# Performance work log

Measured on AMD Instinct MI355X. Metric: run time of the kernel, lower is better.

The kernel has to match this reference:

```python
import jax, jax.numpy as jnp
import numpy as np
from math import sqrt

NOISE_STD = 0.05
ALPHA = 0.2
RHO = 1.0
B, T, I, H, O, R = 64, 2048, 3, 512, 1, 1


def setup_inputs() -> dict:
    key = jax.random.key(0)
    ks = jax.random.split(key, 8)
    return {
        'input': jax.random.normal(ks[0], (B, T, I), dtype=jnp.float32),
        'noise': jax.random.normal(ks[1], (B, T, H), dtype=jnp.float32),
        'w_i': jax.random.normal(ks[2], (I, H), dtype=jnp.float32),
        's_i': jnp.ones((I,), dtype=jnp.float32),
        'm_rec': jax.random.normal(ks[3], (H, R), dtype=jnp.float32),
        'n_rec': jax.random.normal(ks[4], (H, R), dtype=jnp.float32),
        'rec_noise': jax.random.normal(ks[5], (H, H), dtype=jnp.float32) * (RHO / sqrt(H)),
        'w_o': jax.random.normal(ks[6], (H, O), dtype=jnp.float32),
        's_o': jnp.ones((O,), dtype=jnp.float32),
        'h0': jnp.zeros((H,), dtype=jnp.float32),
    }


def reference(input, noise, w_i, s_i, m_rec, n_rec, rec_noise, w_o, s_o, h0):
    hidden = h0.shape[0]
    # proxy parameters (define_proxy_parameters)
    w_rec = m_rec @ n_rec.T / hidden + rec_noise          # [H, H]
    wi_full = w_i * s_i[:, None]                          # [I, H]
    wo_full = w_o * s_o                                   # [H, O]
    # per-step additive drive: noise_std*noise + alpha * (input @ wi_full)
    drive = NOISE_STD * noise + ALPHA * jnp.einsum('bti,ih->bth', input, wi_full)  # [B,T,H]
    h_init = jnp.broadcast_to(h0, (input.shape[0], hidden))

    def step(h, d_t):
        r = jnp.tanh(h)
        h_new = h + d_t + ALPHA * (-h + r @ w_rec.T)
        return h_new, jnp.tanh(h_new)

    _, r_seq = jax.lax.scan(step, h_init, jnp.swapaxes(drive, 0, 1))  # r_seq: [T,B,H]
    output = jnp.einsum('tbh,ho->bto', r_seq, wo_full) / hidden        # [B,T,O]
    return output
```

## Files before the change

kernel.cpp:

```cpp
#include <hip/hip_runtime.h>

constexpr int Bc = 64;
constexpr int Tc = 2048;
constexpr int Ic = 3;
constexpr int Hc = 512;
constexpr float AL = 0.2f;
constexpr float NS = 0.05f;
constexpr int NSL = 4;
constexpr int HS  = Hc / NSL;
constexpr int PAD = 132;

__global__ void prep_wt(const float* __restrict__ m, const float* __restrict__ n,
                        const float* __restrict__ rn, float* __restrict__ WT, int R) {
    int id = blockIdx.x * 256 + threadIdx.x;
    if (id >= Hc * Hc) return;
    int k = id >> 9;
    int h = id & (Hc - 1);
    float acc = rn[h * Hc + k];
    for (int r = 0; r < R; ++r)
        acc = fmaf(m[h * R + r], n[k * R + r] * (1.0f / Hc), acc);
    WT[id] = acc;
}

__device__ __forceinline__ unsigned long long ld_sc0(const unsigned long long* p) {
    unsigned long long v;
    asm volatile("global_load_dwordx2 %0, %1, off sc0\n\t"
                 "s_waitcnt vmcnt(0)"
                 : "=v"(v) : "v"(p) : "memory");
    return v;
}

#define REPEAT32(F) F(0) F(1) F(2) F(3) F(4) F(5) F(6) F(7) \
                    F(8) F(9) F(10) F(11) F(12) F(13) F(14) F(15) \
                    F(16) F(17) F(18) F(19) F(20) F(21) F(22) F(23) \
                    F(24) F(25) F(26) F(27) F(28) F(29) F(30) F(31)

#define WDECL(i) float4 w##i;
#define WLOAD(i) w##i = make_float4(Wp[(size_t)(4*(i)+0) * Hc], \
                                    Wp[(size_t)(4*(i)+1) * Hc], \
                                    Wp[(size_t)(4*(i)+2) * Hc], \
                                    Wp[(size_t)(4*(i)+3) * Hc]);
#define WPIN(i)  asm volatile("" : "+v"(w##i.x), "+v"(w##i.y), "+v"(w##i.z), "+v"(w##i.w));
#define WFMA(i)  { const float4 rv##i = *(const float4*)(rg + 4*(i)); \
                   acc0 = fmaf(w##i.x, rv##i.x, acc0); \
                   acc1 = fmaf(w##i.y, rv##i.y, acc1); \
                   acc2 = fmaf(w##i.z, rv##i.z, acc2); \
                   acc3 = fmaf(w##i.w, rv##i.w, acc3); }

__launch_bounds__(512, 2)
__global__ void rnn4r(const float* __restrict__ input, const float* __restrict__ noise,
                      const float* __restrict__ w_i, const float* __restrict__ s_i,
                      const float* __restrict__ WT, const float* __restrict__ w_o,
                      const float* __restrict__ s_o, const float* __restrict__ h0,
                      float* __restrict__ out, unsigned long long* __restrict__ rbuf) {
    __shared__ float rp[2][NSL * PAD];
    __shared__ float red[8];

    const int tid   = threadIdx.x;
    const int s     = blockIdx.x >> 6;
    const int b     = blockIdx.x & 63;
    const int hl    = tid >> 2;
    const int kg    = tid & 3;
    const int hbase = s * HS;
    const int hmy   = hbase + hl;

    const float* Wp = WT + (size_t)(kg * 128) * Hc + hmy;
    REPEAT32(WDECL)
    REPEAT32(WLOAD)
    REPEAT32(WPIN)

    const float wo_t = w_o[tid] * s_o[0] * (1.0f / Hc);
    float h = h0[hmy];
    const float wi0 = w_i[0 * Hc + hmy] * s_i[0];
    const float wi1 = w_i[1 * Hc + hmy] * s_i[1];
    const float wi2 = w_i[2 * Hc + hmy] * s_i[2];

    rp[0][(tid >> 7) * PAD + (tid & 127)] = tanhf(h0[tid]);

    const float* noise_b = noise + (size_t)b * Tc * Hc;
    const float* inp_b   = input + (size_t)b * Tc * Ic;
    unsigned long long* rb_b = rbuf + (size_t)b * 2 * Hc;

    float nz = noise_b[hmy];
    float i0 = inp_b[0], i1 = inp_b[1], i2 = inp_b[2];

    const int ft   = tid + ((tid >= hbase) ? 128 : 0);
    const int fpos = (ft >> 7) * PAD + (ft & 127);
    __syncthreads();

    for (int t = 0; t < Tc; ++t) {
        const int tn = (t + 1 < Tc) ? t + 1 : t;
        const float nz_n = noise_b[(size_t)tn * Hc + hmy];
        const float i0n = inp_b[tn * Ic + 0];
        const float i1n = inp_b[tn * Ic + 1];
        const float i2n = inp_b[tn * Ic + 2];

        const float* rg = &rp[t & 1][kg * PAD];
        float acc0 = 0.f, acc1 = 0.f, acc2 = 0.f, acc3 = 0.f;
        REPEAT32(WFMA)
        float y = (acc0 + acc1) + (acc2 + acc3);
        y += __shfl_xor(y, 1, 64);
        y += __shfl_xor(y, 2, 64);

        const float di = i0 * wi0 + i1 * wi1 + i2 * wi2;
        h = h + (NS * nz + AL * di) + AL * (y - h);
        const float rv_ = tanhf(h);

        const unsigned want = (unsigned)(t + 1);
        unsigned long long* slot = rb_b + ((size_t)((t + 1) & 1)) * Hc;
        float* wp_ = &rp[(t + 1) & 1][0];

        if (kg == 0) {
            __hip_atomic_store(&slot[hmy],
                               ((unsigned long long)want << 32) |
                               (unsigned long long)__float_as_uint(rv_),
                               __ATOMIC_RELAXED, __HIP_MEMORY_SCOPE_AGENT);
            wp_[s * PAD + hl] = rv_;
        }

        if (tid < 384) {
            const unsigned long long* p = &slot[ft];
            unsigned long long v;
            int it = 0;
            for (;;) {
                if ((it & 3) != 3)
                    v = ld_sc0(p);
                else
                    v = __hip_atomic_load(p, __ATOMIC_RELAXED, __HIP_MEMORY_SCOPE_AGENT);
                if ((unsigned)(v >> 32) == want) break;
                ++it;
            }
            wp_[fpos] = __uint_as_float((unsigned)v);
        }
        __syncthreads();

        if ((t & 3) == s) {
            float p2 = wp_[(tid >> 7) * PAD + (tid & 127)] * wo_t;
            #pragma unroll
            for (int off = 32; off; off >>= 1) p2 += __shfl_xor(p2, off, 64);
            if ((tid & 63) == 0) red[tid >> 6] = p2;
            __syncthreads();
            if (tid == 0)
                out[(size_t)b * Tc + t] = red[0] + red[1] + red[2] + red[3] +
                                          red[4] + red[5] + red[6] + red[7];
        }

        nz = nz_n; i0 = i0n; i1 = i1n; i2 = i2n;
    }
}

__launch_bounds__(512)
__global__ void rnn_scan_fb(const float* __restrict__ input, const float* __restrict__ noise,
                            const float* __restrict__ w_i, const float* __restrict__ s_i,
                            const float* __restrict__ WT, const float* __restrict__ w_o,
                            const float* __restrict__ s_o, const float* __restrict__ h0,
                            float* __restrict__ out) {
    __shared__ float r_lds[Hc];
    __shared__ float pl[4][Hc];
    __shared__ float wi_lds[Ic][Hc];
    __shared__ float red[8];

    const int tid = threadIdx.x;
    const int b   = blockIdx.x;
    const int g   = tid >> 7;
    const int j   = tid & 127;

    for (int i = 0; i < Ic; ++i) wi_lds[i][tid] = w_i[i * Hc + tid] * s_i[i];

    float h = h0[tid];
    float r_cur = tanhf(h);
    const float wo_h = w_o[tid] * s_o[0] * (1.0f / Hc);
    const float* noise_b = noise + (size_t)b * Tc * Hc;
    const float* inp_b   = input + (size_t)b * Tc * Ic;
    float nz = noise_b[tid];
    float i0 = inp_b[0], i1 = inp_b[1], i2 = inp_b[2];
    const float* Wg = WT + (g * 128) * Hc + 4 * j;
    const float* rg = r_lds + g * 128;
    __syncthreads();

    for (int t = 0; t < Tc; ++t) {
        const int tn = (t + 1 < Tc) ? t + 1 : t;
        const float nz_n = noise_b[(size_t)tn * Hc + tid];
        const float i0n = inp_b[tn * Ic + 0];
        const float i1n = inp_b[tn * Ic + 1];
        const float i2n = inp_b[tn * Ic + 2];

        r_lds[tid] = r_cur;
        __syncthreads();
        float a0 = 0.f, a1 = 0.f, a2 = 0.f, a3 = 0.f;
        #pragma unroll 4
        for (int kk = 0; kk < 128; kk += 4) {
            const float4 rv = *(const float4*)(rg + kk);
            const float4 w0 = *(const float4*)(Wg + (kk + 0) * Hc);
            const float4 w1 = *(const float4*)(Wg + (kk + 1) * Hc);
            const float4 w2 = *(const float4*)(Wg + (kk + 2) * Hc);
            const float4 w3 = *(const float4*)(Wg + (kk + 3) * Hc);
            a0 = fmaf(rv.x, w0.x, a0); a0 = fmaf(rv.y, w1.x, a0);
            a0 = fmaf(rv.z, w2.x, a0); a0 = fmaf(rv.w, w3.x, a0);
            a1 = fmaf(rv.x, w0.y, a1); a1 = fmaf(rv.y, w1.y, a1);
            a1 = fmaf(rv.z, w2.y, a1); a1 = fmaf(rv.w, w3.y, a1);
            a2 = fmaf(rv.x, w0.z, a2); a2 = fmaf(rv.y, w1.z, a2);
            a2 = fmaf(rv.z, w2.z, a2); a2 = fmaf(rv.w, w3.z, a2);
            a3 = fmaf(rv.x, w0.w, a3); a3 = fmaf(rv.y, w1.w, a3);
            a3 = fmaf(rv.z, w2.w, a3); a3 = fmaf(rv.w, w3.w, a3);
        }
        *(float4*)&pl[g][4 * j] = make_float4(a0, a1, a2, a3);
        __syncthreads();

        const float y  = pl[0][tid] + pl[1][tid] + pl[2][tid] + pl[3][tid];
        const float di = i0 * wi_lds[0][tid] + i1 * wi_lds[1][tid] + i2 * wi_lds[2][tid];
        h = h + (NS * nz + AL * di) + AL * (y - h);
        r_cur = tanhf(h);

        float p = r_cur * wo_h;
        #pragma unroll
        for (int off = 32; off; off >>= 1) p += __shfl_xor(p, off, 64);
        if ((tid & 63) == 0) red[tid >> 6] = p;
        __syncthreads();
        if (tid == 0)
            out[(size_t)b * Tc + t] = red[0] + red[1] + red[2] + red[3] +
                                      red[4] + red[5] + red[6] + red[7];
        nz = nz_n; i0 = i0n; i1 = i1n; i2 = i2n;
    }
}

extern "C" void kernel_launch(void* const* d_in, const int* in_sizes, int n_in,
                              void* d_out, int out_size, void* d_ws, size_t ws_size,
                              hipStream_t stream) {
    (void)n_in; (void)out_size;
    const float* input     = (const float*)d_in[0];
    const float* noise     = (const float*)d_in[1];
    const float* w_i       = (const float*)d_in[2];
    const float* s_i       = (const float*)d_in[3];
    const float* m_rec     = (const float*)d_in[4];
    const float* n_rec     = (const float*)d_in[5];
    const float* rec_noise = (const float*)d_in[6];
    const float* w_o       = (const float*)d_in[7];
    const float* s_o       = (const float*)d_in[8];
    const float* h0        = (const float*)d_in[9];
    float* out = (float*)d_out;

    const int R = in_sizes[4] / Hc;

    float* WT = (float*)d_ws;
    const size_t wt_bytes = (size_t)Hc * Hc * sizeof(float);
    const size_t rb_bytes = (size_t)Bc * 2 * Hc * sizeof(unsigned long long);

    prep_wt<<<(Hc * Hc + 255) / 256, 256, 0, stream>>>(m_rec, n_rec, rec_noise, WT, R);

    if (ws_size >= wt_bytes + rb_bytes) {
        unsigned long long* rbuf = (unsigned long long*)((char*)d_ws + wt_bytes);
        hipMemsetAsync(rbuf, 0, rb_bytes, stream);
        rnn4r<<<NSL * Bc, 512, 0, stream>>>(input, noise, w_i, s_i, WT, w_o, s_o, h0,
                                            out, rbuf);
    } else {
        rnn_scan_fb<<<Bc, 512, 0, stream>>>(input, noise, w_i, s_i, WT, w_o, s_o, h0, out);
    }
}
```

Baseline: 3.812 ms.

## Split recurrent matvec K dimension across 8 lanes with 1024-thread blocks

Each block now uses 1024 threads, with 8 lanes per hidden unit instead of 4, so each lane holds 64 weights in registers instead of 128 and does half the FMAs per step. The aim is to shorten the per-step critical path of the recurrence and reduce register pressure. The cost is an extra shuffle reduction stage, twice as many waves per barrier, and a reshaped LDS layout with different padding. Occupancy is pinned to 4 waves per EU, which allows one block per CU.

```diff
diff --git a/kernel.cpp b/kernel.cpp
--- a/kernel.cpp
+++ b/kernel.cpp
@@ -7,8 +7,10 @@
 constexpr float AL = 0.2f;
 constexpr float NS = 0.05f;
 constexpr int NSL = 4;
-constexpr int HS  = Hc / NSL;
-constexpr int PAD = 132;
+constexpr int HS  = 128;
+constexpr int KG  = 8;
+constexpr int KS  = 64;
+constexpr int SLP = 68;
 
 __global__ void prep_wt(const float* __restrict__ m, const float* __restrict__ n,
                         const float* __restrict__ rn, float* __restrict__ WT, int R) {
@@ -30,10 +32,8 @@
     return v;
 }
 
-#define REPEAT32(F) F(0) F(1) F(2) F(3) F(4) F(5) F(6) F(7) \
-                    F(8) F(9) F(10) F(11) F(12) F(13) F(14) F(15) \
-                    F(16) F(17) F(18) F(19) F(20) F(21) F(22) F(23) \
-                    F(24) F(25) F(26) F(27) F(28) F(29) F(30) F(31)
+#define REPEAT16(F) F(0) F(1) F(2) F(3) F(4) F(5) F(6) F(7) \
+                    F(8) F(9) F(10) F(11) F(12) F(13) F(14) F(15)
 
 #define WDECL(i) float4 w##i;
 #define WLOAD(i) w##i = make_float4(Wp[(size_t)(4*(i)+0) * Hc], \
@@ -47,35 +47,39 @@
                    acc2 = fmaf(w##i.z, rv##i.z, acc2); \
                    acc3 = fmaf(w##i.w, rv##i.w, acc3); }
 
-__launch_bounds__(512, 2)
-__global__ void rnn4r(const float* __restrict__ input, const float* __restrict__ noise,
-                      const float* __restrict__ w_i, const float* __restrict__ s_i,
-                      const float* __restrict__ WT, const float* __restrict__ w_o,
-                      const float* __restrict__ s_o, const float* __restrict__ h0,
-                      float* __restrict__ out, unsigned long long* __restrict__ rbuf) {
-    __shared__ float rp[2][NSL * PAD];
+__global__ __launch_bounds__(1024)
+__attribute__((amdgpu_waves_per_eu(4, 4)))
+void rnn8g(const float* __restrict__ input, const float* __restrict__ noise,
+           const float* __restrict__ w_i, const float* __restrict__ s_i,
+           const float* __restrict__ WT, const float* __restrict__ w_o,
+           const float* __restrict__ s_o, const float* __restrict__ h0,
+           float* __restrict__ out, unsigned long long* __restrict__ rbuf) {
+    __shared__ __align__(16) float rp[2][KG * SLP];
     __shared__ float red[8];
 
     const int tid   = threadIdx.x;
     const int s     = blockIdx.x >> 6;
     const int b     = blockIdx.x & 63;
-    const int hl    = tid >> 2;
-    const int kg    = tid & 3;
+    const int hl    = tid >> 3;
+    const int kg    = tid & 7;
     const int hbase = s * HS;
     const int hmy   = hbase + hl;
 
-    const float* Wp = WT + (size_t)(kg * 128) * Hc + hmy;
-    REPEAT32(WDECL)
-    REPEAT32(WLOAD)
-    REPEAT32(WPIN)
-
-    const float wo_t = w_o[tid] * s_o[0] * (1.0f / Hc);
+    const float* Wp = WT + (size_t)(kg * KS) * Hc + hmy;
+    REPEAT16(WDECL)
+    REPEAT16(WLOAD)
+    REPEAT16(WPIN)
+
     float h = h0[hmy];
     const float wi0 = w_i[0 * Hc + hmy] * s_i[0];
     const float wi1 = w_i[1 * Hc + hmy] * s_i[1];
     const float wi2 = w_i[2 * Hc + hmy] * s_i[2];
 
-    rp[0][(tid >> 7) * PAD + (tid & 127)] = tanhf(h0[tid]);
+    float wo_t = 0.f;
+    if (tid < Hc) {
+        wo_t = w_o[tid] * s_o[0] * (1.0f / Hc);
+        rp[0][(tid >> 6) * SLP + (tid & 63)] = tanhf(h0[tid]);
+    }
 
     const float* noise_b = noise + (size_t)b * Tc * Hc;
     const float* inp_b   = input + (size_t)b * Tc * Ic;
@@ -84,8 +88,8 @@
     float nz = noise_b[hmy];
     float i0 = inp_b[0], i1 = inp_b[1], i2 = inp_b[2];
 
-    const int ft   = tid + ((tid >= hbase) ? 128 : 0);
-    const int fpos = (ft >> 7) * PAD + (ft & 127);
+    const int ft   = tid + ((tid >= hbase) ? HS : 0);
+    const int fpos = (ft >> 6) * SLP + (ft & 63);
     __syncthreads();
 
     for (int t = 0; t < Tc; ++t) {
@@ -95,12 +99,13 @@
         const float i1n = inp_b[tn * Ic + 1];
         const float i2n = inp_b[tn * Ic + 2];
 
-        const float* rg = &rp[t & 1][kg * PAD];
+        const float* rg = &rp[t & 1][kg * SLP];
         float acc0 = 0.f, acc1 = 0.f, acc2 = 0.f, acc3 = 0.f;
-        REPEAT32(WFMA)
+        REPEAT16(WFMA)
         float y = (acc0 + acc1) + (acc2 + acc3);
         y += __shfl_xor(y, 1, 64);
         y += __shfl_xor(y, 2, 64);
+        y += __shfl_xor(y, 4, 64);
 
         const float di = i0 * wi0 + i1 * wi1 + i2 * wi2;
         h = h + (NS * nz + AL * di) + AL * (y - h);
@@ -115,7 +120,7 @@
                                ((unsigned long long)want << 32) |
                                (unsigned long long)__float_as_uint(rv_),
                                __ATOMIC_RELAXED, __HIP_MEMORY_SCOPE_AGENT);
-            wp_[s * PAD + hl] = rv_;
+            wp_[(hmy >> 6) * SLP + (hmy & 63)] = rv_;
         }
 
         if (tid < 384) {
@@ -135,10 +140,10 @@
         __syncthreads();
 
         if ((t & 3) == s) {
-            float p2 = wp_[(tid >> 7) * PAD + (tid & 127)] * wo_t;
+            float p2 = (tid < Hc) ? wp_[(tid >> 6) * SLP + (tid & 63)] * wo_t : 0.f;
             #pragma unroll
             for (int off = 32; off; off >>= 1) p2 += __shfl_xor(p2, off, 64);
-            if ((tid & 63) == 0) red[tid >> 6] = p2;
+            if (tid < Hc && (tid & 63) == 0) red[tid >> 6] = p2;
             __syncthreads();
             if (tid == 0)
                 out[(size_t)b * Tc + t] = red[0] + red[1] + red[2] + red[3] +
@@ -251,8 +256,8 @@
     if (ws_size >= wt_bytes + rb_bytes) {
         unsigned long long* rbuf = (unsigned long long*)((char*)d_ws + wt_bytes);
         hipMemsetAsync(rbuf, 0, rb_bytes, stream);
-        rnn4r<<<NSL * Bc, 512, 0, stream>>>(input, noise, w_i, s_i, WT, w_o, s_o, h0,
-                                            out, rbuf);
+        rnn8g<<<NSL * Bc, 1024, 0, stream>>>(input, noise, w_i, s_i, WT, w_o, s_o, h0,
+                                             out, rbuf);
     } else {
         rnn_scan_fb<<<Bc, 512, 0, stream>>>(input, noise, w_i, s_i, WT, w_o, s_o, h0, out);
     }
```

After: 4.159 ms. 1.09x slower.
